# Performance work log

Hardware: AMD Instinct MI355X
Metric: run time of the kernel (lower is better)

## Reference

```python
import jax, jax.numpy as jnp
import numpy as np

N_NODES = 8192
N_GRAPHS = 16
KNN_K = 80
N_FEAT = 6
KNN_COLS = (0, 1, 2, 3)
HID = 128
HID6 = 6 * HID
N_LABELS = 3
BN_EPS = 1e-5


def knn_edges(pos, batch, k):
    # pos: [N, 4]; batch: [N] graph ids. Returns (src, tgt) with k neighbors per node,
    # restricted to same graph, excluding self (PyG knn_graph, flow source_to_target).
    n = pos.shape[0]
    sq = jnp.sum(pos * pos, axis=1)
    d2 = sq[:, None] + sq[None, :] - 2.0 * (pos @ pos.T)  # [N, N]
    valid = (batch[:, None] == batch[None, :]) & ~jnp.eye(n, dtype=bool)
    d2 = jnp.where(valid, d2, jnp.inf)
    _, idx = jax.lax.top_k(-d2, k)  # k smallest distances per row
    src = idx.reshape(-1)                      # neighbor j (message source)
    tgt = jnp.repeat(jnp.arange(n), k)         # center node i (message target)
    return src, tgt


def tag_conv(x, src, tgt, norm, W, b):
    # TAGConv K=2: out = sum_k (A_hat^k x) W_k + b, A_hat = D^-1/2 A D^-1/2
    n = x.shape[0]
    out = x @ W[0]
    h = x
    for k in range(1, W.shape[0]):
        h = jax.ops.segment_sum(norm[:, None] * h[src], tgt, num_segments=n)
        out = out + h @ W[k]
    return out + b


def pool_mean_max(x, batch, n_graphs):
    cnt = jax.ops.segment_sum(jnp.ones((x.shape[0],), x.dtype), batch, num_segments=n_graphs)
    mean = jax.ops.segment_sum(x, batch, num_segments=n_graphs) / cnt[:, None]
    mx = jax.ops.segment_max(x, batch, num_segments=n_graphs)
    return jnp.concatenate([mean, mx], axis=1)


def setup_inputs() -> dict:
    key = jax.random.key(0)
    ks = jax.random.split(key, 16)
    x = jax.random.normal(ks[0], (N_NODES, N_FEAT), dtype=jnp.float32)
    batch = jnp.repeat(jnp.arange(N_GRAPHS, dtype=jnp.int32), N_NODES // N_GRAPHS)
    s1 = 1.0 / np.sqrt(N_FEAT)
    s2 = 1.0 / np.sqrt(HID)
    s3 = 1.0 / np.sqrt(HID6)
    return {
        "x": x,
        "batch": batch,
        "conv1_w": jax.random.uniform(ks[1], (3, N_FEAT, HID), jnp.float32, -s1, s1),
        "conv1_b": jnp.zeros((HID,), jnp.float32),
        "conv2_w": jax.random.uniform(ks[2], (3, HID, HID), jnp.float32, -s2, s2),
        "conv2_b": jnp.zeros((HID,), jnp.float32),
        "conv3_w": jax.random.uniform(ks[3], (3, HID, HID), jnp.float32, -s2, s2),
        "conv3_b": jnp.zeros((HID,), jnp.float32),
        "bn_gamma": jnp.ones((HID6,), jnp.float32),
        "bn_beta": jnp.zeros((HID6,), jnp.float32),
        "bn_mean": 0.1 * jax.random.normal(ks[4], (HID6,), jnp.float32),
        "bn_var": jax.random.uniform(ks[5], (HID6,), jnp.float32, 0.5, 1.5),
        "lin_w": jax.random.uniform(ks[6], (5, HID6, HID6), jnp.float32, -s3, s3),
        "lin_b": jax.random.uniform(ks[7], (5, HID6), jnp.float32, -s3, s3),
        "out_w": jax.random.uniform(ks[8], (HID6, N_LABELS), jnp.float32, -s3, s3),
        "out_b": jax.random.uniform(ks[9], (N_LABELS,), jnp.float32, -s3, s3),
    }


def reference(x, batch, conv1_w, conv1_b, conv2_w, conv2_b, conv3_w, conv3_b,
              bn_gamma, bn_beta, bn_mean, bn_var, lin_w, lin_b, out_w, out_b):
    n = x.shape[0]
    pos = x[:, jnp.array(KNN_COLS)]
    src, tgt = knn_edges(pos, batch, KNN_K)
    # gcn_norm without self loops (edge dropout disabled: eval-mode determinism)
    deg = jax.ops.segment_sum(jnp.ones_like(src, dtype=x.dtype), tgt, num_segments=n)
    dinv = jnp.where(deg > 0, jax.lax.rsqrt(jnp.maximum(deg, 1.0)), 0.0)
    norm = dinv[src] * dinv[tgt]

    h = jax.nn.leaky_relu(tag_conv(x, src, tgt, norm, conv1_w, conv1_b))
    p1 = pool_mean_max(h, batch, N_GRAPHS)
    h = jax.nn.leaky_relu(tag_conv(h, src, tgt, norm, conv2_w, conv2_b))
    p2 = pool_mean_max(h, batch, N_GRAPHS)
    h = jax.nn.leaky_relu(tag_conv(h, src, tgt, norm, conv3_w, conv3_b))
    p3 = pool_mean_max(h, batch, N_GRAPHS)

    g = jnp.concatenate([p1, p2, p3], axis=1)  # [B, 768]
    g = (g - bn_mean) * jax.lax.rsqrt(bn_var + BN_EPS) * bn_gamma + bn_beta
    for i in range(lin_w.shape[0]):
        g = jax.nn.leaky_relu(g @ lin_w[i] + lin_b[i])
    out = g @ out_w + out_b
    return out.reshape(-1, N_LABELS)
```

## Files before the change

kernel.cpp:

```cpp
#include <hip/hip_runtime.h>

constexpr int N    = 8192;
constexpr int NPG  = 512;
constexpr int NG   = 16;
constexpr int KNN  = 80;
constexpr int F0   = 6;
constexpr int HID  = 128;
constexpr int H6   = 768;
constexpr int RPB  = 16;
constexpr int BPGR = NPG / RPB;
constexpr size_t SPLIT_STRIDE = (size_t)NG * HID * NPG;

typedef _Float16 half8 __attribute__((ext_vector_type(8)));
typedef float    f32x4 __attribute__((ext_vector_type(4)));

__device__ __forceinline__ float leaky(float v) { return v > 0.0f ? v : 0.01f * v; }

__device__ __forceinline__ int lanes_below(unsigned long long m) {
    return __builtin_amdgcn_mbcnt_hi((unsigned)(m >> 32),
           __builtin_amdgcn_mbcnt_lo((unsigned)m, 0));
}

__device__ __forceinline__ int wave_count_sum(int c) {
    int total = 0;
    #pragma unroll
    for (int b = 0; b < 4; b++)
        total += (int)__popcll(__ballot((c >> b) & 1)) << b;
    return total;
}

__global__ __launch_bounds__(256) void knn_kernel(const float* __restrict__ x,
                                                  int* __restrict__ nbr,
                                                  _Float16* __restrict__ Aadj) {
    constexpr int BPG = 128;
    const int tid  = threadIdx.x;
    const int lane = tid & 63;
    const int wv   = tid >> 6;
    const int base = (blockIdx.x / BPG) << 9;
    const int t    = base + (blockIdx.x & (BPG - 1)) * 4 + wv;
    const int tl   = t - base;

    __shared__ float px[512], py[512], pz[512], pw[512];
    __shared__ unsigned long long skey[4 * 128];

    {
        const uint4 z = {0u, 0u, 0u, 0u};
        *(uint4*)(Aadj + (size_t)t * 512 + lane * 8) = z;
    }

    for (int j = tid; j < 512; j += 256) {
        const float* row = x + (size_t)(base + j) * F0;
        const float2 ra = *(const float2*)(row);
        const float2 rb = *(const float2*)(row + 2);
        px[j] = ra.x; py[j] = ra.y; pz[j] = rb.x; pw[j] = rb.y;
    }
    __syncthreads();

    const float tx = px[tl], ty = py[tl], tz = pz[tl], tw = pw[tl];
    const float sqt = tx*tx + ty*ty + tz*tz + tw*tw;

    unsigned d2m[8];
    #pragma unroll
    for (int j = 0; j < 8; j++) {
        const int node = j * 64 + lane;
        const float jx = px[node], jy = py[node], jz = pz[node], jw = pw[node];
        const float sqj = jx*jx + jy*jy + jz*jz + jw*jw;
        const float dot = tx*jx + ty*jy + tz*jz + tw*jw;
        const float d2  = sqt + sqj - 2.0f * dot;
        unsigned u = __float_as_uint(d2);
        u = (u & 0x80000000u) ? ~u : (u | 0x80000000u);
        d2m[j] = (node == tl) ? 0xFFFFFFFFu : u;
    }

    unsigned V = 0;
    for (int b = 31; b >= 0; --b) {
        const unsigned test = V | (1u << b);
        int c = 0;
        #pragma unroll
        for (int j = 0; j < 8; j++) c += (d2m[j] < test) ? 1 : 0;
        if (wave_count_sum(c) < KNN) V = test;
    }

    int c = 0;
    #pragma unroll
    for (int j = 0; j < 8; j++) c += (d2m[j] < V) ? 1 : 0;
    const int n_lt = wave_count_sum(c);
    const int need = KNN - n_lt;

    const int woff = wv * 128;
    int cnt_total = 0, taken = 0;
    #pragma unroll
    for (int j = 0; j < 8; j++) {
        const bool lt = d2m[j] < V;
        const bool eq = d2m[j] == V;
        const unsigned long long meq = __ballot(eq);
        const bool sel = lt || (eq && (taken + lanes_below(meq)) < need);
        taken += (int)__popcll(meq);
        const unsigned long long msel = __ballot(sel);
        if (sel) {
            const int pos = cnt_total + lanes_below(msel);
            skey[woff + pos] = ((unsigned long long)d2m[j] << 32)
                             | (unsigned)(base + j * 64 + lane);
        }
        cnt_total += (int)__popcll(msel);
    }
    for (int i = KNN + lane; i < 128; i += 64) skey[woff + i] = ~0ULL;
    __syncthreads();

    for (int kk = 2; kk <= 128; kk <<= 1) {
        for (int jj = kk >> 1; jj >= 1; jj >>= 1) {
            const int i  = ((lane & ~(jj - 1)) << 1) | (lane & (jj - 1));
            const int ix = i | jj;
            const unsigned long long a = skey[woff + i];
            const unsigned long long b = skey[woff + ix];
            const bool up = ((i & kk) == 0);
            if ((a > b) == up) { skey[woff + i] = b; skey[woff + ix] = a; }
            __syncthreads();
        }
    }

    if (lane < KNN) {
        const int idx = (int)(unsigned)skey[woff + lane];
        nbr[t * KNN + lane] = idx;
        Aadj[(size_t)t * 512 + (idx & 511)] = (_Float16)1.0f;
    }
    if (lane + 64 < KNN) {
        const int idx = (int)(unsigned)skey[woff + lane + 64];
        nbr[t * KNN + lane + 64] = idx;
        Aadj[(size_t)t * 512 + (idx & 511)] = (_Float16)1.0f;
    }
}

__global__ __launch_bounds__(256) void prop6(const float* __restrict__ hin,
                                             const int* __restrict__ nbr,
                                             float* __restrict__ hout) {
    const int t = blockIdx.x * 256 + threadIdx.x;
    if (t >= N) return;
    const int* nb = nbr + t * KNN;
    float a0=0.f,a1=0.f,a2=0.f,a3=0.f,a4=0.f,a5=0.f;
    for (int i = 0; i < KNN; i += 4) {
        const int4 s4 = *(const int4*)(nb + i);
        {   const float* r = hin + (size_t)s4.x * F0;
            a0+=r[0]; a1+=r[1]; a2+=r[2]; a3+=r[3]; a4+=r[4]; a5+=r[5]; }
        {   const float* r = hin + (size_t)s4.y * F0;
            a0+=r[0]; a1+=r[1]; a2+=r[2]; a3+=r[3]; a4+=r[4]; a5+=r[5]; }
        {   const float* r = hin + (size_t)s4.z * F0;
            a0+=r[0]; a1+=r[1]; a2+=r[2]; a3+=r[3]; a4+=r[4]; a5+=r[5]; }
        {   const float* r = hin + (size_t)s4.w * F0;
            a0+=r[0]; a1+=r[1]; a2+=r[2]; a3+=r[3]; a4+=r[4]; a5+=r[5]; }
    }
    const float inv = 1.0f / 80.0f;
    float* o = hout + (size_t)t * F0;
    o[0]=a0*inv; o[1]=a1*inv; o[2]=a2*inv; o[3]=a3*inv; o[4]=a4*inv; o[5]=a5*inv;
}

__global__ __launch_bounds__(256) void split_kernel(const float* __restrict__ H,
                                                    _Float16* __restrict__ Bout) {
    __shared__ unsigned tt[128][67];
    const int tid = threadIdx.x;
    const int n0  = blockIdx.x * 64;
    const int g   = n0 >> 9;
    const int nl  = n0 & 511;

    #pragma unroll
    for (int q = 0; q < 8; q++) {
        const int i  = tid + q * 256;
        const int n  = i >> 5;
        const int c4 = (i & 31) * 4;
        const float4 v = *(const float4*)(H + ((size_t)(n0 + n)) * HID + c4);
        const float fr[4] = {v.x, v.y, v.z, v.w};
        #pragma unroll
        for (int e = 0; e < 4; e++) {
            const float f = fr[e];
            const _Float16 h1 = (_Float16)f;
            const _Float16 h2 = (_Float16)(f - (float)h1);
            tt[c4 + e][n] = ((unsigned)__builtin_bit_cast(unsigned short, h2) << 16)
                          |  (unsigned)__builtin_bit_cast(unsigned short, h1);
        }
    }
    __syncthreads();

    const int c  = tid >> 1;
    const int jh = tid & 1;
    _Float16 o1[32], o2[32];
    #pragma unroll
    for (int s = 0; s < 32; s++) {
        const unsigned u = tt[c][jh * 32 + s];
        o1[s] = __builtin_bit_cast(_Float16, (unsigned short)(u & 0xFFFFu));
        o2[s] = __builtin_bit_cast(_Float16, (unsigned short)(u >> 16));
    }
    _Float16* d1 = Bout + ((size_t)g * HID + c) * NPG + nl + jh * 32;
    _Float16* d2 = d1 + SPLIT_STRIDE;
    #pragma unroll
    for (int q = 0; q < 4; q++) {
        *(uint4*)(d1 + q * 8) = *(const uint4*)&o1[q * 8];
        *(uint4*)(d2 + q * 8) = *(const uint4*)&o2[q * 8];
    }
}

template<bool EMIT>
__global__ __launch_bounds__(128) void hop_kernel(const _Float16* __restrict__ A,
                                                  const _Float16* __restrict__ Bin,
                                                  float* __restrict__ Y,
                                                  _Float16* __restrict__ Bout) {
    __shared__ _Float16 Bs[2][128][72];
    __shared__ float Ct[32][132];

    const int tid  = threadIdx.x;
    const int lane = tid & 63;
    const int w    = tid >> 6;
    const int g    = blockIdx.x >> 4;
    const int m0   = (blockIdx.x & 15) * 32;

    f32x4 acc[8];
    #pragma unroll
    for (int j = 0; j < 8; j++) acc[j] = {0.f, 0.f, 0.f, 0.f};

    const _Float16* Arow = A + ((size_t)(g * 512 + m0 + w * 16 + (lane & 15))) * 512;
    const int klane = (lane >> 4) * 8;
    const int stg_c = tid >> 3;
    const int stg_o = (tid & 7) * 8;

    for (int ch = 0; ch < 8; ch++) {
        const int k0 = ch * 64;
        #pragma unroll
        for (int s = 0; s < 2; s++) {
            const _Float16* src = Bin + (size_t)s * SPLIT_STRIDE
                                + (size_t)g * HID * NPG + k0;
            #pragma unroll
            for (int it = 0; it < 8; it++) {
                const int cc = stg_c + it * 16;
                const uint4 v = *(const uint4*)(src + (size_t)cc * NPG + stg_o);
                *(uint4*)&Bs[s][cc][stg_o] = v;
            }
        }
        __syncthreads();
        #pragma unroll
        for (int ks = 0; ks < 2; ks++) {
            const half8 af = *(const half8*)(Arow + k0 + ks * 32 + klane);
            #pragma unroll
            for (int s = 0; s < 2; s++) {
                #pragma unroll
                for (int j = 0; j < 8; j++) {
                    const half8 bf = *(const half8*)&Bs[s][j * 16 + (lane & 15)][ks * 32 + klane];
                    acc[j] = __builtin_amdgcn_mfma_f32_16x16x32_f16(af, bf, acc[j], 0, 0, 0);
                }
            }
        }
        __syncthreads();
    }

    const float inv = 1.0f / 80.0f;
    {
        const int rbase = w * 16 + (lane >> 4) * 4;
        const int c0 = lane & 15;
        #pragma unroll
        for (int j = 0; j < 8; j++)
            #pragma unroll
            for (int rg = 0; rg < 4; rg++)
                Ct[rbase + rg][j * 16 + c0] = acc[j][rg] * inv;
    }
    __syncthreads();

    #pragma unroll
    for (int q = 0; q < 8; q++) {
        const int i  = tid + q * 128;
        const int r  = i >> 5;
        const int c4 = (i & 31) * 4;
        const float4 v = *(const float4*)&Ct[r][c4];
        *(float4*)(Y + ((size_t)(g * 512 + m0 + r)) * HID + c4) = v;
    }

    if (EMIT) {
        const int c = tid;
        _Float16 o1[32], o2[32];
        #pragma unroll
        for (int k = 0; k < 32; k++) {
            const float v = Ct[k][c];
            const _Float16 h1 = (_Float16)v;
            o1[k] = h1;
            o2[k] = (_Float16)(v - (float)h1);
        }
        _Float16* d1 = Bout + ((size_t)g * HID + c) * NPG + m0;
        _Float16* d2 = d1 + SPLIT_STRIDE;
        #pragma unroll
        for (int q = 0; q < 4; q++) {
            *(uint4*)(d1 + q * 8) = *(const uint4*)&o1[q * 8];
            *(uint4*)(d2 + q * 8) = *(const uint4*)&o2[q * 8];
        }
    }
}

template<int K>
__global__ __launch_bounds__(256) void combine_kernel(const float* __restrict__ X,
                                                      const float* __restrict__ Y1,
                                                      const float* __restrict__ Y2,
                                                      const float* __restrict__ W,
                                                      const float* __restrict__ bias,
                                                      float* __restrict__ out,
                                                      float* __restrict__ psum,
                                                      float* __restrict__ pmax) {
    __shared__ float xs[3][RPB * K];
    const int tid  = threadIdx.x;
    const int row0 = blockIdx.x * RPB;

    {
        const float* s0 = X  + (size_t)row0 * K;
        const float* s1 = Y1 + (size_t)row0 * K;
        const float* s2 = Y2 + (size_t)row0 * K;
        if constexpr ((K & 3) == 0) {
            constexpr int NV = RPB * K / 4;
            for (int i = tid; i < NV; i += 256) ((float4*)xs[0])[i] = ((const float4*)s0)[i];
            for (int i = tid; i < NV; i += 256) ((float4*)xs[1])[i] = ((const float4*)s1)[i];
            for (int i = tid; i < NV; i += 256) ((float4*)xs[2])[i] = ((const float4*)s2)[i];
        } else {
            for (int i = tid; i < RPB * K; i += 256) xs[0][i] = s0[i];
            for (int i = tid; i < RPB * K; i += 256) xs[1][i] = s1[i];
            for (int i = tid; i < RPB * K; i += 256) xs[2][i] = s2[i];
        }
    }
    __syncthreads();

    const int c  = tid & 127;
    const int r0 = (tid >> 7) * 8;

    float acc[8];
    #pragma unroll
    for (int r = 0; r < 8; r++) acc[r] = 0.0f;

    #pragma unroll
    for (int s = 0; s < 3; s++) {
        const float* __restrict__ Ws   = W + (size_t)s * K * HID;
        const float* __restrict__ xseg = xs[s] + r0 * K;
        for (int k = 0; k < K; k += 2) {
            const float w0 = Ws[(size_t)k * HID + c];
            const float w1 = Ws[(size_t)(k + 1) * HID + c];
            #pragma unroll
            for (int r = 0; r < 8; r++)
                acc[r] += xseg[r * K + k] * w0 + xseg[r * K + k + 1] * w1;
        }
    }

    const float bb = bias[c];
    float sum8 = 0.0f, mx8 = -3.402823e38f;
    #pragma unroll
    for (int r = 0; r < 8; r++) {
        const float v = leaky(acc[r] + bb);
        out[(size_t)(row0 + r0 + r) * HID + c] = v;
        sum8 += v;
        mx8 = fmaxf(mx8, v);
    }

    __shared__ float ssum[128], smx[128];
    if (r0) { ssum[c] = sum8; smx[c] = mx8; }
    __syncthreads();
    if (!r0) {
        psum[(size_t)blockIdx.x * HID + c] = sum8 + ssum[c];
        pmax[(size_t)blockIdx.x * HID + c] = fmaxf(mx8, smx[c]);
    }
}

__global__ __launch_bounds__(128) void pool2_kernel(const float* __restrict__ psum,
                                                    const float* __restrict__ pmax,
                                                    float* __restrict__ g, int conv) {
    const int gr = blockIdx.x;
    const int c  = threadIdx.x;
    float s = 0.0f, m = -3.402823e38f;
    const float* ps = psum + (size_t)gr * BPGR * HID + c;
    const float* pm = pmax + (size_t)gr * BPGR * HID + c;
    #pragma unroll 8
    for (int b = 0; b < BPGR; b++) {
        s += ps[b * HID];
        m = fmaxf(m, pm[b * HID]);
    }
    float* grow = g + (size_t)gr * H6 + conv * 256;
    grow[c]       = s * (1.0f / 512.0f);
    grow[128 + c] = m;
}

template<bool BN>
__global__ __launch_bounds__(256) void lin_kernel(const float* __restrict__ gin,
                                                  const float* __restrict__ W,
                                                  const float* __restrict__ bias,
                                                  float* __restrict__ gout,
                                                  const float* __restrict__ gamma,
                                                  const float* __restrict__ beta,
                                                  const float* __restrict__ mean,
                                                  const float* __restrict__ var) {
    const int r   = blockIdx.x / 6;
    const int cc  = blockIdx.x % 6;
    const int tid = threadIdx.x;

    __shared__ float gs[H6];
    for (int k = tid; k < H6; k += 256) {
        float v = gin[(size_t)r * H6 + k];
        if (BN) v = (v - mean[k]) * (1.0f / sqrtf(var[k] + 1e-5f)) * gamma[k] + beta[k];
        gs[k] = v;
    }
    __syncthreads();

    const int c  = cc * 128 + (tid & 127);
    const int kh = tid >> 7;
    const int kb = kh * 384;
    float a0=0.f,a1=0.f,a2=0.f,a3=0.f;
    for (int k = kb; k < kb + 384; k += 4) {
        a0 += gs[k]     * W[(size_t)(k)     * H6 + c];
        a1 += gs[k + 1] * W[(size_t)(k + 1) * H6 + c];
        a2 += gs[k + 2] * W[(size_t)(k + 2) * H6 + c];
        a3 += gs[k + 3] * W[(size_t)(k + 3) * H6 + c];
    }
    __shared__ float part[256];
    part[tid] = (a0 + a1) + (a2 + a3);
    __syncthreads();
    if (kh == 0) {
        const float v = part[tid] + part[tid + 128] + bias[c];
        gout[(size_t)r * H6 + c] = leaky(v);
    }
}

__global__ void out_kernel(const float* __restrict__ gin,
                           const float* __restrict__ W,
                           const float* __restrict__ bias,
                           float* __restrict__ out) {
    const int tid = threadIdx.x;
    __shared__ float part[192];
    if (tid < 192) {
        const int q  = tid >> 2;
        const int r  = q / 3, c = q % 3;
        const int kq = tid & 3;
        float acc = 0.0f;
        for (int k = kq * 192; k < kq * 192 + 192; k++)
            acc += gin[(size_t)r * H6 + k] * W[(size_t)k * 3 + c];
        part[tid] = acc;
    }
    __syncthreads();
    if (tid < 48) {
        const int r = tid / 3, c = tid % 3;
        out[r * 3 + c] = part[tid*4] + part[tid*4+1] + part[tid*4+2] + part[tid*4+3] + bias[c];
    }
}

extern "C" void kernel_launch(void* const* d_in, const int* in_sizes, int n_in,
                              void* d_out, int out_size, void* d_ws, size_t ws_size,
                              hipStream_t stream) {
    const float* x        = (const float*)d_in[0];
    const float* conv1_w  = (const float*)d_in[2];
    const float* conv1_b  = (const float*)d_in[3];
    const float* conv2_w  = (const float*)d_in[4];
    const float* conv2_b  = (const float*)d_in[5];
    const float* conv3_w  = (const float*)d_in[6];
    const float* conv3_b  = (const float*)d_in[7];
    const float* bn_gamma = (const float*)d_in[8];
    const float* bn_beta  = (const float*)d_in[9];
    const float* bn_mean  = (const float*)d_in[10];
    const float* bn_var   = (const float*)d_in[11];
    const float* lin_w    = (const float*)d_in[12];
    const float* lin_b    = (const float*)d_in[13];
    const float* out_w    = (const float*)d_in[14];
    const float* out_b    = (const float*)d_in[15];

    char* ws = (char*)d_ws;
    size_t off = 0;
    auto alloc = [&](size_t bytes) {
        void* p = ws + off;
        off += (bytes + 255) & ~(size_t)255;
        return p;
    };
    int*      nbr  = (int*)      alloc((size_t)N * KNN * 4);
    float*    y6a  = (float*)    alloc((size_t)N * F0 * 4);
    float*    y6b  = (float*)    alloc((size_t)N * F0 * 4);
    float*    hA   = (float*)    alloc((size_t)N * HID * 4);
    float*    hB   = (float*)    alloc((size_t)N * HID * 4);
    float*    y1   = (float*)    alloc((size_t)N * HID * 4);
    float*    y2   = (float*)    alloc((size_t)N * HID * 4);
    float*    ga   = (float*)    alloc((size_t)NG * H6 * 4);
    float*    gb   = (float*)    alloc((size_t)NG * H6 * 4);
    float*    psum = (float*)    alloc((size_t)(N / RPB) * HID * 4);
    float*    pmax = (float*)    alloc((size_t)(N / RPB) * HID * 4);
    _Float16* Aadj = (_Float16*) alloc((size_t)N * NPG * 2);
    _Float16* Sa   = (_Float16*) alloc(2 * SPLIT_STRIDE * 2);
    _Float16* Sb   = (_Float16*) alloc(2 * SPLIT_STRIDE * 2);

    knn_kernel<<<N / 4, 256, 0, stream>>>(x, nbr, Aadj);

    prop6<<<N / 256, 256, 0, stream>>>(x, nbr, y6a);
    prop6<<<N / 256, 256, 0, stream>>>(y6a, nbr, y6b);
    combine_kernel<6><<<N / RPB, 256, 0, stream>>>(x, y6a, y6b, conv1_w, conv1_b, hA, psum, pmax);
    pool2_kernel<<<NG, 128, 0, stream>>>(psum, pmax, ga, 0);

    split_kernel<<<N / 64, 256, 0, stream>>>(hA, Sa);
    hop_kernel<true ><<<NG * 16, 128, 0, stream>>>(Aadj, Sa, y1, Sb);
    hop_kernel<false><<<NG * 16, 128, 0, stream>>>(Aadj, Sb, y2, nullptr);
    combine_kernel<128><<<N / RPB, 256, 0, stream>>>(hA, y1, y2, conv2_w, conv2_b, hB, psum, pmax);
    pool2_kernel<<<NG, 128, 0, stream>>>(psum, pmax, ga, 1);

    split_kernel<<<N / 64, 256, 0, stream>>>(hB, Sa);
    hop_kernel<true ><<<NG * 16, 128, 0, stream>>>(Aadj, Sa, y1, Sb);
    hop_kernel<false><<<NG * 16, 128, 0, stream>>>(Aadj, Sb, y2, nullptr);
    combine_kernel<128><<<N / RPB, 256, 0, stream>>>(hB, y1, y2, conv3_w, conv3_b, hA, psum, pmax);
    pool2_kernel<<<NG, 128, 0, stream>>>(psum, pmax, ga, 2);

    lin_kernel<true ><<<96, 256, 0, stream>>>(ga, lin_w + 0 * H6 * H6, lin_b + 0 * H6, gb,
                                              bn_gamma, bn_beta, bn_mean, bn_var);
    lin_kernel<false><<<96, 256, 0, stream>>>(gb, lin_w + 1 * H6 * H6, lin_b + 1 * H6, ga,
                                              nullptr, nullptr, nullptr, nullptr);
    lin_kernel<false><<<96, 256, 0, stream>>>(ga, lin_w + 2 * H6 * H6, lin_b + 2 * H6, gb,
                                              nullptr, nullptr, nullptr, nullptr);
    lin_kernel<false><<<96, 256, 0, stream>>>(gb, lin_w + 3 * H6 * H6, lin_b + 3 * H6, ga,
                                              nullptr, nullptr, nullptr, nullptr);
    lin_kernel<false><<<96, 256, 0, stream>>>(ga, lin_w + 4 * H6 * H6, lin_b + 4 * H6, gb,
                                              nullptr, nullptr, nullptr, nullptr);
    out_kernel<<<1, 256, 0, stream>>>(gb, out_w, out_b, (float*)d_out);
}
```

Before: 307.5 us.

## Retile hop GEMM into small per-wave tiles reading operands directly from global

The dense per-graph adjacency GEMM is reorganised from 32x128 output tiles per block, with the B operand staged through shared memory, into 16x64 tiles per 256-thread block where each wave computes one 16x16 tile and loads A and B fragments straight from global memory. Grid size grows from 256 to 1024 blocks, which gives better occupancy across the many compute units and removes the per-chunk shared-memory staging and barriers. In exchange, A and B fragments are reloaded by many more blocks with no reuse through LDS, so global and L2 traffic rise. The fp16 hi/lo split output is written in smaller 8-byte chunks.

Result: slower. 334.4 us (+8.8%).

```diff
diff --git a/kernel.cpp b/kernel.cpp
--- a/kernel.cpp
+++ b/kernel.cpp
@@ -199,95 +199,69 @@
 }
 
 template<bool EMIT>
-__global__ __launch_bounds__(128) void hop_kernel(const _Float16* __restrict__ A,
+__global__ __launch_bounds__(256) void hop_kernel(const _Float16* __restrict__ A,
                                                   const _Float16* __restrict__ Bin,
                                                   float* __restrict__ Y,
                                                   _Float16* __restrict__ Bout) {
-    __shared__ _Float16 Bs[2][128][72];
-    __shared__ float Ct[32][132];
+    __shared__ float Ct[16][68];
 
     const int tid  = threadIdx.x;
     const int lane = tid & 63;
     const int w    = tid >> 6;
-    const int g    = blockIdx.x >> 4;
-    const int m0   = (blockIdx.x & 15) * 32;
-
-    f32x4 acc[8];
-    #pragma unroll
-    for (int j = 0; j < 8; j++) acc[j] = {0.f, 0.f, 0.f, 0.f};
-
-    const _Float16* Arow = A + ((size_t)(g * 512 + m0 + w * 16 + (lane & 15))) * 512;
-    const int klane = (lane >> 4) * 8;
-    const int stg_c = tid >> 3;
-    const int stg_o = (tid & 7) * 8;
-
-    for (int ch = 0; ch < 8; ch++) {
-        const int k0 = ch * 64;
-        #pragma unroll
-        for (int s = 0; s < 2; s++) {
-            const _Float16* src = Bin + (size_t)s * SPLIT_STRIDE
-                                + (size_t)g * HID * NPG + k0;
-            #pragma unroll
-            for (int it = 0; it < 8; it++) {
-                const int cc = stg_c + it * 16;
-                const uint4 v = *(const uint4*)(src + (size_t)cc * NPG + stg_o);
-                *(uint4*)&Bs[s][cc][stg_o] = v;
-            }
-        }
-        __syncthreads();
-        #pragma unroll
-        for (int ks = 0; ks < 2; ks++) {
-            const half8 af = *(const half8*)(Arow + k0 + ks * 32 + klane);
-            #pragma unroll
-            for (int s = 0; s < 2; s++) {
-                #pragma unroll
-                for (int j = 0; j < 8; j++) {
-                    const half8 bf = *(const half8*)&Bs[s][j * 16 + (lane & 15)][ks * 32 + klane];
-                    acc[j] = __builtin_amdgcn_mfma_f32_16x16x32_f16(af, bf, acc[j], 0, 0, 0);
-                }
-            }
-        }
-        __syncthreads();
+    const int rt   = blockIdx.x >> 1;
+    const int h    = blockIdx.x & 1;
+    const int g    = rt >> 5;
+
+    const int row = rt * 16 + (lane & 15);
+    const int col = h * 64 + w * 16 + (lane & 15);
+    const int kl  = (lane >> 4) * 8;
+
+    const _Float16* Ap = A   + (size_t)row * 512 + kl;
+    const _Float16* B0 = Bin + ((size_t)g * HID + col) * NPG + kl;
+    const _Float16* B1 = B0 + SPLIT_STRIDE;
+
+    f32x4 acc = {0.f, 0.f, 0.f, 0.f};
+    #pragma unroll 8
+    for (int ks = 0; ks < 16; ks++) {
+        const half8 af = *(const half8*)(Ap + ks * 32);
+        const half8 b0 = *(const half8*)(B0 + ks * 32);
+        const half8 b1 = *(const half8*)(B1 + ks * 32);
+        acc = __builtin_amdgcn_mfma_f32_16x16x32_f16(af, b0, acc, 0, 0, 0);
+        acc = __builtin_amdgcn_mfma_f32_16x16x32_f16(af, b1, acc, 0, 0, 0);
     }
 
     const float inv = 1.0f / 80.0f;
     {
-        const int rbase = w * 16 + (lane >> 4) * 4;
-        const int c0 = lane & 15;
+        const int rbase = (lane >> 4) * 4;
+        const int cc    = w * 16 + (lane & 15);
         #pragma unroll
-        for (int j = 0; j < 8; j++)
-            #pragma unroll
-            for (int rg = 0; rg < 4; rg++)
-                Ct[rbase + rg][j * 16 + c0] = acc[j][rg] * inv;
-    }
-    __syncthreads();
-
-    #pragma unroll
-    for (int q = 0; q < 8; q++) {
-        const int i  = tid + q * 128;
-        const int r  = i >> 5;
-        const int c4 = (i & 31) * 4;
+        for (int rg = 0; rg < 4; rg++)
+            Ct[rbase + rg][cc] = acc[rg] * inv;
+    }
+    __syncthreads();
+
+    {
+        const int r  = tid >> 4;
+        const int c4 = (tid & 15) * 4;
         const float4 v = *(const float4*)&Ct[r][c4];
-        *(float4*)(Y + ((size_t)(g * 512 + m0 + r)) * HID + c4) = v;
+        *(float4*)(Y + ((size_t)(rt * 16 + r)) * HID + h * 64 + c4) = v;
     }
 
     if (EMIT) {
-        const int c = tid;
-        _Float16 o1[32], o2[32];
+        const int cl = tid >> 2;
+        const int nq = tid & 3;
+        _Float16 o1[4], o2[4];
         #pragma unroll
-        for (int k = 0; k < 32; k++) {
-            const float v = Ct[k][c];
-            const _Float16 h1 = (_Float16)v;
-            o1[k] = h1;
-            o2[k] = (_Float16)(v - (float)h1);
-        }
-        _Float16* d1 = Bout + ((size_t)g * HID + c) * NPG + m0;
+        for (int i = 0; i < 4; i++) {
+            const float v = Ct[nq * 4 + i][cl];
+            o1[i] = (_Float16)v;
+            o2[i] = (_Float16)(v - (float)o1[i]);
+        }
+        const int nl0 = (rt * 16) & 511;
+        _Float16* d1 = Bout + ((size_t)g * HID + h * 64 + cl) * NPG + nl0 + nq * 4;
         _Float16* d2 = d1 + SPLIT_STRIDE;
-        #pragma unroll
-        for (int q = 0; q < 4; q++) {
-            *(uint4*)(d1 + q * 8) = *(const uint4*)&o1[q * 8];
-            *(uint4*)(d2 + q * 8) = *(const uint4*)&o2[q * 8];
-        }
+        *(uint2*)d1 = *(const uint2*)o1;
+        *(uint2*)d2 = *(const uint2*)o2;
     }
 }
 
@@ -489,14 +463,14 @@
     pool2_kernel<<<NG, 128, 0, stream>>>(psum, pmax, ga, 0);
 
     split_kernel<<<N / 64, 256, 0, stream>>>(hA, Sa);
-    hop_kernel<true ><<<NG * 16, 128, 0, stream>>>(Aadj, Sa, y1, Sb);
-    hop_kernel<false><<<NG * 16, 128, 0, stream>>>(Aadj, Sb, y2, nullptr);
+    hop_kernel<true ><<<N / 16 * 2, 256, 0, stream>>>(Aadj, Sa, y1, Sb);
+    hop_kernel<false><<<N / 16 * 2, 256, 0, stream>>>(Aadj, Sb, y2, nullptr);
     combine_kernel<128><<<N / RPB, 256, 0, stream>>>(hA, y1, y2, conv2_w, conv2_b, hB, psum, pmax);
     pool2_kernel<<<NG, 128, 0, stream>>>(psum, pmax, ga, 1);
 
     split_kernel<<<N / 64, 256, 0, stream>>>(hB, Sa);
-    hop_kernel<true ><<<NG * 16, 128, 0, stream>>>(Aadj, Sa, y1, Sb);
-    hop_kernel<false><<<NG * 16, 128, 0, stream>>>(Aadj, Sb, y2, nullptr);
+    hop_kernel<true ><<<N / 16 * 2, 256, 0, stream>>>(Aadj, Sa, y1, Sb);
+    hop_kernel<false><<<N / 16 * 2, 256, 0, stream>>>(Aadj, Sb, y2, nullptr);
     combine_kernel<128><<<N / RPB, 256, 0, stream>>>(hB, y1, y2, conv3_w, conv3_b, hA, psum, pmax);
     pool2_kernel<<<NG, 128, 0, stream>>>(psum, pmax, ga, 2);
 
```
